# Performance work log

Hardware: AMD Instinct MI355X
Metric: run time of the kernel (lower is better)

## Reference

```python
import jax, jax.numpy as jnp
import numpy as np


def setup_inputs() -> dict:
    key = jax.random.key(0)
    k1, k2, k3 = jax.random.split(key, 3)
    B, S, D = 4, 4096, 2048
    a = jax.random.uniform(k1, (B, S, D), dtype=jnp.float32)   # decay coeffs in [0,1)
    b = jax.random.normal(k2, (B, S, D), dtype=jnp.float32)
    h0 = jax.random.normal(k3, (B, D), dtype=jnp.float32)
    return {"a": a, "b": b, "h0": h0}


def _scan(a, b):
    # Associative op for h_t = a_t * h_{t-1} + b_t:
    # combining left segment (a_l, b_l) then right segment (a_r, b_r)
    # gives (a_l * a_r, a_r * b_l + b_r).
    def combine(left, right):
        a_l, b_l = left
        a_r, b_r = right
        return a_l * a_r, a_r * b_l + b_r
    _, h = jax.lax.associative_scan(combine, (a, b), axis=1)
    return h  # (batch, seq_len, dim)


def reference(a, b, h0):
    # Fold initial state into first input term: b_0 <- b_0 + a_0 * h0
    b = b.at[:, 0, :].add(a[:, 0, :] * h0)
    return _scan(a, b)
```

## Files before the change

kernel.cpp:

```cpp
#include <hip/hip_runtime.h>

#define BATCH 4
#define SEQ   4096
#define DIM   2048
#define NC    128
#define LSEG  (SEQ / NC)
#define D4    (DIM / 4)
#define GQ    2
#define NBLK  (BATCH * GQ * NC)
#define NCHAIN (BATCH * DIM)

__global__ __launch_bounds__(256) void k1_aggregate(
    const float4* __restrict__ a4, const float4* __restrict__ b4,
    float4* __restrict__ aggA4, float4* __restrict__ aggB4)
{
    const int tid = threadIdx.x;
    const int bx = blockIdx.x;
    const int c     = bx & (NC - 1);
    const int r     = bx >> 7;
    const int batch = r >> 1;
    const int gq    = r & 1;
    const int d4    = gq * 256 + tid;

    unsigned base = (unsigned)(batch * SEQ + c * LSEG) * D4 + d4;

    float4 A = make_float4(1.f, 1.f, 1.f, 1.f);
    float4 B = make_float4(0.f, 0.f, 0.f, 0.f);
#pragma unroll 8
    for (int t = 0; t < LSEG; ++t) {
        const float4 av = a4[base + (unsigned)t * D4];
        const float4 bv = b4[base + (unsigned)t * D4];
        B.x = fmaf(av.x, B.x, bv.x);  A.x *= av.x;
        B.y = fmaf(av.y, B.y, bv.y);  A.y *= av.y;
        B.z = fmaf(av.z, B.z, bv.z);  A.z *= av.z;
        B.w = fmaf(av.w, B.w, bv.w);  A.w *= av.w;
    }
    const unsigned aidx = (unsigned)c * (NCHAIN / 4) + batch * (DIM / 4) + d4;
    aggA4[aidx] = A;
    aggB4[aidx] = B;
}

__global__ __launch_bounds__(256) void k2_scan_agg(
    const float* __restrict__ aggA, const float* __restrict__ aggB,
    const float* __restrict__ h0, float* __restrict__ pref)
{
    const int ch = blockIdx.x * 256 + threadIdx.x;
    float h = h0[ch];
#pragma unroll 8
    for (int c = 0; c < NC; ++c) {
        const unsigned idx = (unsigned)c * NCHAIN + ch;
        pref[idx] = h;
        h = fmaf(aggA[idx], h, aggB[idx]);
    }
}

__global__ __launch_bounds__(256) void k3_apply(
    const float4* __restrict__ a4, const float4* __restrict__ b4,
    const float4* __restrict__ pref4, float4* __restrict__ out4)
{
    const int tid = threadIdx.x;
    const int bx = blockIdx.x;
    const int c     = bx & (NC - 1);
    const int r     = bx >> 7;
    const int batch = r >> 1;
    const int gq    = r & 1;
    const int d4    = gq * 256 + tid;

    unsigned base = (unsigned)(batch * SEQ + c * LSEG) * D4 + d4;
    const unsigned aidx = (unsigned)c * (NCHAIN / 4) + batch * (DIM / 4) + d4;

    float4 h = pref4[aidx];
#pragma unroll 8
    for (int t = 0; t < LSEG; ++t) {
        const float4 av = a4[base + (unsigned)t * D4];
        const float4 bv = b4[base + (unsigned)t * D4];
        h.x = fmaf(av.x, h.x, bv.x);
        h.y = fmaf(av.y, h.y, bv.y);
        h.z = fmaf(av.z, h.z, bv.z);
        h.w = fmaf(av.w, h.w, bv.w);
        out4[base + (unsigned)t * D4] = h;
    }
}

__global__ void scan_naive_kernel(
    const float* __restrict__ a, const float* __restrict__ b,
    const float* __restrict__ h0, float* __restrict__ out)
{
    const int chain = blockIdx.x * blockDim.x + threadIdx.x;
    if (chain >= NCHAIN) return;
    const int batch = chain / DIM;
    const int dim = chain % DIM;
    float h = h0[batch * DIM + dim];
    unsigned idx = (unsigned)(batch * SEQ) * DIM + dim;
    for (int s = 0; s < SEQ; ++s, idx += DIM) {
        h = fmaf(a[idx], h, b[idx]);
        out[idx] = h;
    }
}

extern "C" void kernel_launch(void* const* d_in, const int* in_sizes, int n_in,
                              void* d_out, int out_size, void* d_ws, size_t ws_size,
                              hipStream_t stream) {
    const float* a  = (const float*)d_in[0];
    const float* b  = (const float*)d_in[1];
    const float* h0 = (const float*)d_in[2];
    float* out = (float*)d_out;

    const size_t seg_vals = (size_t)NC * NCHAIN;
    const size_t need = 3 * seg_vals * sizeof(float);

    if (ws_size >= need) {
        float* aggA = (float*)d_ws;
        float* aggB = aggA + seg_vals;
        float* pref = aggB + seg_vals;

        k1_aggregate<<<dim3(NBLK), dim3(256), 0, stream>>>(
            (const float4*)a, (const float4*)b, (float4*)aggA, (float4*)aggB);
        k2_scan_agg<<<dim3(NCHAIN / 256), dim3(256), 0, stream>>>(
            aggA, aggB, h0, pref);
        k3_apply<<<dim3(NBLK), dim3(256), 0, stream>>>(
            (const float4*)a, (const float4*)b, (const float4*)pref, (float4*)out);
    } else {
        scan_naive_kernel<<<dim3((NCHAIN + 255) / 256), dim3(256), 0, stream>>>(
            a, b, h0, out);
    }
}
```

Before: 381.3 us.

## Shorten scan segments, parallelize carry scan, batch loads and use nontemporal stores

Segments shrink to 16 steps when workspace allows, doubling the block count in the aggregate and apply passes to raise parallelism. The carry scan now splits each chain's chunks across 8 thread groups with a shared-memory second-level scan. Loads of a and b are batched 8 at a time to expose memory-level parallelism, and output stores are nontemporal. Shorter segments double the aggregate and prefix workspace traffic, and the new code depends on the harness providing enough workspace.

```diff
diff --git a/kernel.cpp b/kernel.cpp
--- a/kernel.cpp
+++ b/kernel.cpp
@@ -3,82 +3,127 @@
 #define BATCH 4
 #define SEQ   4096
 #define DIM   2048
-#define NC    128
-#define LSEG  (SEQ / NC)
 #define D4    (DIM / 4)
 #define GQ    2
-#define NBLK  (BATCH * GQ * NC)
 #define NCHAIN (BATCH * DIM)
 
+typedef __attribute__((ext_vector_type(4))) float v4f;
+
+template<int LSEG>
 __global__ __launch_bounds__(256) void k1_aggregate(
     const float4* __restrict__ a4, const float4* __restrict__ b4,
     float4* __restrict__ aggA4, float4* __restrict__ aggB4)
 {
-    const int tid = threadIdx.x;
-    const int bx = blockIdx.x;
-    const int c     = bx & (NC - 1);
-    const int r     = bx >> 7;
-    const int batch = r >> 1;
-    const int gq    = r & 1;
-    const int d4    = gq * 256 + tid;
+    const int c     = blockIdx.x;
+    const int gq    = blockIdx.y;
+    const int batch = blockIdx.z;
+    const int d4    = gq * 256 + threadIdx.x;
 
     unsigned base = (unsigned)(batch * SEQ + c * LSEG) * D4 + d4;
 
     float4 A = make_float4(1.f, 1.f, 1.f, 1.f);
     float4 B = make_float4(0.f, 0.f, 0.f, 0.f);
-#pragma unroll 8
-    for (int t = 0; t < LSEG; ++t) {
-        const float4 av = a4[base + (unsigned)t * D4];
-        const float4 bv = b4[base + (unsigned)t * D4];
-        B.x = fmaf(av.x, B.x, bv.x);  A.x *= av.x;
-        B.y = fmaf(av.y, B.y, bv.y);  A.y *= av.y;
-        B.z = fmaf(av.z, B.z, bv.z);  A.z *= av.z;
-        B.w = fmaf(av.w, B.w, bv.w);  A.w *= av.w;
+
+#pragma unroll 1
+    for (int h = 0; h < LSEG / 8; ++h) {
+        float4 av[8], bv[8];
+        const unsigned hb = base + (unsigned)(h * 8) * D4;
+#pragma unroll
+        for (int i = 0; i < 8; ++i) av[i] = a4[hb + (unsigned)i * D4];
+#pragma unroll
+        for (int i = 0; i < 8; ++i) bv[i] = b4[hb + (unsigned)i * D4];
+#pragma unroll
+        for (int i = 0; i < 8; ++i) {
+            B.x = fmaf(av[i].x, B.x, bv[i].x);  A.x *= av[i].x;
+            B.y = fmaf(av[i].y, B.y, bv[i].y);  A.y *= av[i].y;
+            B.z = fmaf(av[i].z, B.z, bv[i].z);  A.z *= av[i].z;
+            B.w = fmaf(av[i].w, B.w, bv[i].w);  A.w *= av[i].w;
+        }
     }
     const unsigned aidx = (unsigned)c * (NCHAIN / 4) + batch * (DIM / 4) + d4;
     aggA4[aidx] = A;
     aggB4[aidx] = B;
 }
 
-__global__ __launch_bounds__(256) void k2_scan_agg(
+template<int NC>
+__global__ __launch_bounds__(512) void k2_scan_agg(
     const float* __restrict__ aggA, const float* __restrict__ aggB,
     const float* __restrict__ h0, float* __restrict__ pref)
 {
-    const int ch = blockIdx.x * 256 + threadIdx.x;
-    float h = h0[ch];
+    constexpr int CPG = NC / 8;
+    const int lc = threadIdx.x & 63;
+    const int g  = threadIdx.x >> 6;
+    const int ch = blockIdx.x * 64 + lc;
+
+    const unsigned idx0 = (unsigned)(g * CPG) * NCHAIN + (unsigned)ch;
+
+    float A = 1.f, B = 0.f;
 #pragma unroll 8
-    for (int c = 0; c < NC; ++c) {
-        const unsigned idx = (unsigned)c * NCHAIN + ch;
+    for (int i = 0; i < CPG; ++i) {
+        const unsigned idx = idx0 + (unsigned)i * NCHAIN;
+        const float a = aggA[idx];
+        const float b = aggB[idx];
+        B = fmaf(a, B, b);
+        A *= a;
+    }
+
+    __shared__ float sA[8][64];
+    __shared__ float sB[8][64];
+    __shared__ float sH[8][64];
+    sA[g][lc] = A;
+    sB[g][lc] = B;
+    __syncthreads();
+
+    if (threadIdx.x < 64) {
+        float h = h0[ch];
+#pragma unroll
+        for (int j = 0; j < 8; ++j) {
+            sH[j][lc] = h;
+            h = fmaf(sA[j][lc], h, sB[j][lc]);
+        }
+    }
+    __syncthreads();
+
+    float h = sH[g][lc];
+#pragma unroll 8
+    for (int i = 0; i < CPG; ++i) {
+        const unsigned idx = idx0 + (unsigned)i * NCHAIN;
         pref[idx] = h;
         h = fmaf(aggA[idx], h, aggB[idx]);
     }
 }
 
+template<int LSEG>
 __global__ __launch_bounds__(256) void k3_apply(
     const float4* __restrict__ a4, const float4* __restrict__ b4,
     const float4* __restrict__ pref4, float4* __restrict__ out4)
 {
-    const int tid = threadIdx.x;
-    const int bx = blockIdx.x;
-    const int c     = bx & (NC - 1);
-    const int r     = bx >> 7;
-    const int batch = r >> 1;
-    const int gq    = r & 1;
-    const int d4    = gq * 256 + tid;
+    const int c     = blockIdx.x;
+    const int gq    = blockIdx.y;
+    const int batch = blockIdx.z;
+    const int d4    = gq * 256 + threadIdx.x;
 
     unsigned base = (unsigned)(batch * SEQ + c * LSEG) * D4 + d4;
     const unsigned aidx = (unsigned)c * (NCHAIN / 4) + batch * (DIM / 4) + d4;
 
     float4 h = pref4[aidx];
-#pragma unroll 8
-    for (int t = 0; t < LSEG; ++t) {
-        const float4 av = a4[base + (unsigned)t * D4];
-        const float4 bv = b4[base + (unsigned)t * D4];
-        h.x = fmaf(av.x, h.x, bv.x);
-        h.y = fmaf(av.y, h.y, bv.y);
-        h.z = fmaf(av.z, h.z, bv.z);
-        h.w = fmaf(av.w, h.w, bv.w);
-        out4[base + (unsigned)t * D4] = h;
+
+#pragma unroll 1
+    for (int hh = 0; hh < LSEG / 8; ++hh) {
+        float4 av[8], bv[8];
+        const unsigned hb = base + (unsigned)(hh * 8) * D4;
+#pragma unroll
+        for (int i = 0; i < 8; ++i) av[i] = a4[hb + (unsigned)i * D4];
+#pragma unroll
+        for (int i = 0; i < 8; ++i) bv[i] = b4[hb + (unsigned)i * D4];
+#pragma unroll
+        for (int i = 0; i < 8; ++i) {
+            h.x = fmaf(av[i].x, h.x, bv[i].x);
+            h.y = fmaf(av[i].y, h.y, bv[i].y);
+            h.z = fmaf(av[i].z, h.z, bv[i].z);
+            h.w = fmaf(av[i].w, h.w, bv[i].w);
+            __builtin_nontemporal_store(*(const v4f*)&h, (v4f*)&out4[hb + (unsigned)i * D4]);
+        }
     }
 }
 
@@ -98,6 +143,24 @@
     }
 }
 
+template<int LSEG>
+static void run_path(const float* a, const float* b, const float* h0,
+                     float* out, float* ws, hipStream_t stream)
+{
+    constexpr int NC = SEQ / LSEG;
+    const size_t seg_vals = (size_t)NC * NCHAIN;
+    float* aggA = ws;
+    float* aggB = aggA + seg_vals;
+    float* pref = aggB + seg_vals;
+
+    k1_aggregate<LSEG><<<dim3(NC, GQ, BATCH), dim3(256), 0, stream>>>(
+        (const float4*)a, (const float4*)b, (float4*)aggA, (float4*)aggB);
+    k2_scan_agg<NC><<<dim3(NCHAIN / 64), dim3(512), 0, stream>>>(
+        aggA, aggB, h0, pref);
+    k3_apply<LSEG><<<dim3(NC, GQ, BATCH), dim3(256), 0, stream>>>(
+        (const float4*)a, (const float4*)b, (const float4*)pref, (float4*)out);
+}
+
 extern "C" void kernel_launch(void* const* d_in, const int* in_sizes, int n_in,
                               void* d_out, int out_size, void* d_ws, size_t ws_size,
                               hipStream_t stream) {
@@ -106,20 +169,13 @@
     const float* h0 = (const float*)d_in[2];
     float* out = (float*)d_out;
 
-    const size_t seg_vals = (size_t)NC * NCHAIN;
-    const size_t need = 3 * seg_vals * sizeof(float);
+    const size_t need16 = 3 * (size_t)(SEQ / 16) * NCHAIN * sizeof(float);
+    const size_t need32 = 3 * (size_t)(SEQ / 32) * NCHAIN * sizeof(float);
 
-    if (ws_size >= need) {
-        float* aggA = (float*)d_ws;
-        float* aggB = aggA + seg_vals;
-        float* pref = aggB + seg_vals;
-
-        k1_aggregate<<<dim3(NBLK), dim3(256), 0, stream>>>(
-            (const float4*)a, (const float4*)b, (float4*)aggA, (float4*)aggB);
-        k2_scan_agg<<<dim3(NCHAIN / 256), dim3(256), 0, stream>>>(
-            aggA, aggB, h0, pref);
-        k3_apply<<<dim3(NBLK), dim3(256), 0, stream>>>(
-            (const float4*)a, (const float4*)b, (const float4*)pref, (float4*)out);
+    if (ws_size >= need16) {
+        run_path<16>(a, b, h0, out, (float*)d_ws, stream);
+    } else if (ws_size >= need32) {
+        run_path<32>(a, b, h0, out, (float*)d_ws, stream);
     } else {
         scan_naive_kernel<<<dim3((NCHAIN + 255) / 256), dim3(256), 0, stream>>>(
             a, b, h0, out);
```

Result: faster. 369.3 us (-3.1%).
